# Kernel tuning notes

Hardware: AMD Instinct MI355X
Metric: run time of the kernel (lower is better)

## Reference

```python
import jax, jax.numpy as jnp
import numpy as np

N_NODES = 100000
N_EDGES = 3200000
N_FEAT = 128
DIM = 64
N_GRAPHS = 4096
EPS = 1e-5


def setup_inputs() -> dict:
    key = jax.random.key(0)
    ks = jax.random.split(key, 20)
    x = jax.random.normal(ks[0], (N_NODES, N_FEAT), dtype=jnp.float32)
    edge_index = jax.random.randint(ks[1], (2, N_EDGES), 0, N_NODES, dtype=jnp.int64)
    batch = jnp.sort(jax.random.randint(ks[2], (N_NODES,), 0, N_GRAPHS, dtype=jnp.int64))
    s = 0.1
    inp = {
        "x": x, "edge_index": edge_index, "batch": batch,
        "w1": jax.random.normal(ks[3], (N_FEAT, DIM), jnp.float32) * s,
        "b1": jnp.zeros((DIM,), jnp.float32),
        "bn1_g": 1.0 + s * jax.random.normal(ks[4], (DIM,), jnp.float32),
        "bn1_b": s * jax.random.normal(ks[5], (DIM,), jnp.float32),
        "conv_w": jax.random.normal(ks[6], (3, DIM, DIM), jnp.float32) * s,
        "conv_b": jnp.zeros((3, DIM), jnp.float32),
        "bnc_g": 1.0 + s * jax.random.normal(ks[7], (3, DIM), jnp.float32),
        "bnc_b": s * jax.random.normal(ks[8], (3, DIM), jnp.float32),
        "mlp_w": jax.random.normal(ks[9], (3, DIM, DIM), jnp.float32) * s,
        "mlp_b": jnp.zeros((3, DIM), jnp.float32),
        "bnm_g": 1.0 + s * jax.random.normal(ks[10], (3, DIM), jnp.float32),
        "bnm_b": s * jax.random.normal(ks[11], (3, DIM), jnp.float32),
        "out_w": jax.random.normal(ks[12], (DIM, 1), jnp.float32) * s,
        "out_b": jnp.zeros((1,), jnp.float32),
    }
    return inp


def _batchnorm(h, g, b):
    # training-mode BN: batch stats over the node/graph axis, biased variance
    m = jnp.mean(h, axis=0)
    v = jnp.var(h, axis=0)
    return (h - m) * jax.lax.rsqrt(v + EPS) * g + b


def _forward(x, edge_index, batch, w1, b1, bn1_g, bn1_b, conv_w, conv_b,
             bnc_g, bnc_b, mlp_w, mlp_b, bnm_g, bnm_b, out_w, out_b):
    src, dst = edge_index[0], edge_index[1]
    n = x.shape[0]
    # degree with self-loops (GCNConv default: add_self_loops=True, sym norm)
    deg = jax.ops.segment_sum(jnp.ones((src.shape[0],), x.dtype), dst, num_segments=n) + 1.0
    dis = jax.lax.rsqrt(deg)                  # D^{-1/2}
    enorm = (dis[src] * dis[dst])[:, None]    # per-edge norm [E,1]
    self_norm = (dis * dis)[:, None]          # self-loop norm = 1/deg [N,1]

    def gcn(h, W, b):
        h = h @ W                                                  # lin first (PyG)
        agg = jax.ops.segment_sum(h[src] * enorm, dst, num_segments=n)
        return agg + h * self_norm + b

    h = _batchnorm(jax.nn.relu(gcn(x, w1, b1)), bn1_g, bn1_b)
    for i in range(3):
        h = _batchnorm(gcn(h, conv_w[i], conv_b[i]), bnc_g[i], bnc_b[i])
    p = jax.ops.segment_sum(h, batch, num_segments=N_GRAPHS)       # global_add_pool
    for i in range(3):
        p = _batchnorm(jax.nn.relu(p @ mlp_w[i] + mlp_b[i]), bnm_g[i], bnm_b[i])
        # dropout: eval mode -> identity
    return p @ out_w + out_b


def reference(x, edge_index, batch, w1, b1, bn1_g, bn1_b, conv_w, conv_b,
              bnc_g, bnc_b, mlp_w, mlp_b, bnm_g, bnm_b, out_w, out_b):
    return _forward(x, edge_index, batch, w1, b1, bn1_g, bn1_b, conv_w, conv_b,
                    bnc_g, bnc_b, mlp_w, mlp_b, bnm_g, bnm_b, out_w, out_b)
```

## Files before the change

### kernel.cpp

```cpp
#include <hip/hip_runtime.h>
#include <hip/hip_bf16.h>

#define N_FEAT 128
#define DIM 64


__global__ void hist_kernel(const int* __restrict__ dst, int E, int* __restrict__ cnt) {
    int e = blockIdx.x * blockDim.x + threadIdx.x;
    if (e < E) atomicAdd(&cnt[dst[e]], 1);
}

__global__ void dis_kernel(const int* __restrict__ cnt, float* __restrict__ dis, int N) {
    int i = blockIdx.x * blockDim.x + threadIdx.x;
    if (i < N) dis[i] = rsqrtf((float)cnt[i] + 1.0f);
}

__global__ void scanA_kernel(const int* __restrict__ cnt, int N,
                             int* __restrict__ tmp, int* __restrict__ blk) {
    __shared__ int ts[256];
    int t = threadIdx.x;
    int base = blockIdx.x * 1024 + t * 4;
    int v[4];
    int s = 0;
#pragma unroll
    for (int j = 0; j < 4; j++) {
        int i = base + j;
        v[j] = (i < N) ? cnt[i] : 0;
        s += v[j];
    }
    ts[t] = s;
    __syncthreads();
    for (int off = 1; off < 256; off <<= 1) {
        int x = (t >= off) ? ts[t - off] : 0;
        __syncthreads();
        ts[t] += x;
        __syncthreads();
    }
    int run = ts[t] - s;
#pragma unroll
    for (int j = 0; j < 4; j++) {
        run += v[j];
        int i = base + j;
        if (i < N) tmp[i] = run;
    }
    if (t == 255) blk[blockIdx.x] = ts[255];
}

__global__ void scanB_kernel(int* __restrict__ blk, int nb) {
    __shared__ int ts[128];
    int t = threadIdx.x;
    int v = (t < nb) ? blk[t] : 0;
    ts[t] = v;
    __syncthreads();
    for (int off = 1; off < 128; off <<= 1) {
        int x = (t >= off) ? ts[t - off] : 0;
        __syncthreads();
        ts[t] += x;
        __syncthreads();
    }
    if (t < nb) blk[t] = ts[t] - v;
}

__global__ void scanC_kernel(const int* __restrict__ tmp, const int* __restrict__ blk,
                             int N, int E, int* __restrict__ rowp, int* __restrict__ cur) {
    int i = blockIdx.x * blockDim.x + threadIdx.x;
    if (i < N) {
        int b = i >> 10;
        int local = i & 1023;
        int excl = blk[b] + (local ? tmp[i - 1] : 0);
        rowp[i] = excl;
        cur[i] = excl;
    }
    if (i == 0) rowp[N] = E;
}

__global__ void fill_kernel(const int* __restrict__ src, const int* __restrict__ dst, int E,
                            const float* __restrict__ dis, int* __restrict__ cur,
                            int2* __restrict__ ecw) {
    int e = blockIdx.x * blockDim.x + threadIdx.x;
    if (e < E) {
        int s = src[e], d = dst[e];
        int pos = atomicAdd(&cur[d], 1);
        ecw[pos] = make_int2(s, __float_as_int(dis[s] * dis[d]));
    }
}


template<int K, bool AFFINE, bool BIAS, bool RELU, bool STATS>
__global__ __launch_bounds__(256) void gemm_kernel(
    const float* __restrict__ A, const float* __restrict__ W,
    const float* __restrict__ scale, const float* __restrict__ shift,
    const float* __restrict__ bias, float* __restrict__ C,
    float* __restrict__ stats, int M)
{
    __shared__ float As[64][K + 1];
    __shared__ float Ws[K][64];
    __shared__ float bs[64], bq[64];
    int t = threadIdx.x;
    int row0 = blockIdx.x * 64;

    for (int q = t; q < K * 16; q += 256) {
        int k = q >> 4, c4 = (q & 15) << 2;
        float4 w = *reinterpret_cast<const float4*>(&W[k * 64 + c4]);
        *reinterpret_cast<float4*>(&Ws[k][c4]) = w;
    }
    for (int q = t; q < 64 * (K / 4); q += 256) {
        int r = q / (K / 4);
        int k4 = (q % (K / 4)) * 4;
        int row = row0 + r;
        float4 a;
        if (row < M) {
            a = *reinterpret_cast<const float4*>(&A[(size_t)row * K + k4]);
            if (AFFINE) {
                a.x = a.x * scale[k4]     + shift[k4];
                a.y = a.y * scale[k4 + 1] + shift[k4 + 1];
                a.z = a.z * scale[k4 + 2] + shift[k4 + 2];
                a.w = a.w * scale[k4 + 3] + shift[k4 + 3];
            }
        } else {
            a = make_float4(0.f, 0.f, 0.f, 0.f);
        }
        As[r][k4] = a.x; As[r][k4 + 1] = a.y; As[r][k4 + 2] = a.z; As[r][k4 + 3] = a.w;
    }
    __syncthreads();

    int ty = t >> 4, tx = t & 15;
    int r0 = ty * 4, c0 = tx * 4;
    float acc[4][4] = {};
#pragma unroll 8
    for (int k = 0; k < K; k++) {
        float a0 = As[r0][k], a1 = As[r0 + 1][k], a2 = As[r0 + 2][k], a3 = As[r0 + 3][k];
        float4 w = *reinterpret_cast<const float4*>(&Ws[k][c0]);
        acc[0][0] += a0 * w.x; acc[0][1] += a0 * w.y; acc[0][2] += a0 * w.z; acc[0][3] += a0 * w.w;
        acc[1][0] += a1 * w.x; acc[1][1] += a1 * w.y; acc[1][2] += a1 * w.z; acc[1][3] += a1 * w.w;
        acc[2][0] += a2 * w.x; acc[2][1] += a2 * w.y; acc[2][2] += a2 * w.z; acc[2][3] += a2 * w.w;
        acc[3][0] += a3 * w.x; acc[3][1] += a3 * w.y; acc[3][2] += a3 * w.z; acc[3][3] += a3 * w.w;
    }

    if (STATS) {
        if (t < 64) { bs[t] = 0.f; bq[t] = 0.f; }
        __syncthreads();
    }
    float ssum[4] = {0.f, 0.f, 0.f, 0.f}, ssq[4] = {0.f, 0.f, 0.f, 0.f};
#pragma unroll
    for (int i = 0; i < 4; i++) {
        int row = row0 + r0 + i;
        if (row < M) {
            float4 v;
            float* vp = &v.x;
#pragma unroll
            for (int j = 0; j < 4; j++) {
                float x = acc[i][j];
                if (BIAS) x += bias[c0 + j];
                if (RELU) x = fmaxf(x, 0.f);
                vp[j] = x;
                if (STATS) { ssum[j] += x; ssq[j] += x * x; }
            }
            *reinterpret_cast<float4*>(&C[(size_t)row * 64 + c0]) = v;
        }
    }
    if (STATS) {
#pragma unroll
        for (int j = 0; j < 4; j++) {
            atomicAdd(&bs[c0 + j], ssum[j]);
            atomicAdd(&bq[c0 + j], ssq[j]);
        }
        __syncthreads();
        if (t < 64) {
            atomicAdd(&stats[t], bs[t]);
            atomicAdd(&stats[64 + t], bq[t]);
        }
    }
}


template<bool RELU>
__global__ __launch_bounds__(256) void agg_kernel(
    const float* __restrict__ H, const int* __restrict__ rowp,
    const int2* __restrict__ ecw,
    const float* __restrict__ dis, const float* __restrict__ bias,
    float* __restrict__ Hout, float* __restrict__ stats, int N)
{
    __shared__ float bs[64], bq[64];
    int t = threadIdx.x;
    int lane = t & 63;
    int base = (blockIdx.x * 4 + (t >> 6)) * 8;
    float b = bias[lane];
    float ssum = 0.f, ssq = 0.f;
    for (int u = 0; u < 8; u++) {
        int n = base + u;
        if (n >= N) break;
        int e0 = rowp[n], e1 = rowp[n + 1];
        float acc = 0.f;
        for (int e = e0; e < e1; e += 8) {
            int   idx[8];
            float ww[8];
#pragma unroll
            for (int j = 0; j < 8; j++) {
                int ee = e + j;
                bool ok = ee < e1;
                int2 p = ecw[ok ? ee : e0];
                idx[j] = p.x;
                ww[j]  = ok ? __int_as_float(p.y) : 0.f;
            }
            float h[8];
#pragma unroll
            for (int j = 0; j < 8; j++)
                h[j] = H[(size_t)idx[j] * 64 + lane];
#pragma unroll
            for (int j = 0; j < 8; j++)
                acc += h[j] * ww[j];
        }
        float dn = dis[n];
        acc += H[(size_t)n * 64 + lane] * (dn * dn);
        acc += b;
        if (RELU) acc = fmaxf(acc, 0.f);
        Hout[(size_t)n * 64 + lane] = acc;
        ssum += acc;
        ssq += acc * acc;
    }
    if (t < 64) { bs[t] = 0.f; bq[t] = 0.f; }
    __syncthreads();
    atomicAdd(&bs[lane], ssum);
    atomicAdd(&bq[lane], ssq);
    __syncthreads();
    if (t < 64) {
        atomicAdd(&stats[t], bs[t]);
        atomicAdd(&stats[64 + t], bq[t]);
    }
}


__global__ void bnprep_kernel(const float* __restrict__ stats, const float* __restrict__ g,
                              const float* __restrict__ b, float* __restrict__ ss, float cntInv) {
    int c = threadIdx.x;
    float mean = stats[c] * cntInv;
    float var = stats[64 + c] * cntInv - mean * mean;
    float sc = g[c] * rsqrtf(var + 1e-5f);
    ss[c] = sc;
    ss[64 + c] = b[c] - mean * sc;
}


__global__ __launch_bounds__(256) void pool_kernel(
    const float* __restrict__ H, const int* __restrict__ batch,
    const float* __restrict__ ss, float* __restrict__ P, int N)
{
    int t = threadIdx.x;
    int lane = t & 63;
    int base = (blockIdx.x * 4 + (t >> 6)) * 8;
    float sc = ss[lane], sh = ss[64 + lane];
    float acc = 0.f;
    int gprev = -1;
    for (int u = 0; u < 8; u++) {
        int n = base + u;
        if (n >= N) break;
        int g = batch[n];
        if (g != gprev) {
            if (gprev >= 0) atomicAdd(&P[(size_t)gprev * 64 + lane], acc);
            acc = 0.f;
            gprev = g;
        }
        acc += H[(size_t)n * 64 + lane] * sc + sh;
    }
    if (gprev >= 0) atomicAdd(&P[(size_t)gprev * 64 + lane], acc);
}


__global__ __launch_bounds__(256) void final_kernel(
    const float* __restrict__ P, const float* __restrict__ ss,
    const float* __restrict__ outw, const float* __restrict__ outb,
    float* __restrict__ out, int G)
{
    int t = threadIdx.x;
    int lane = t & 63;
    int g = blockIdx.x * 4 + (t >> 6);
    if (g >= G) return;
    float v = (P[(size_t)g * 64 + lane] * ss[lane] + ss[64 + lane]) * outw[lane];
#pragma unroll
    for (int off = 32; off >= 1; off >>= 1) v += __shfl_xor(v, off, 64);
    if (lane == 0) out[g] = v + outb[0];
}


extern "C" void kernel_launch(void* const* d_in, const int* in_sizes, int n_in,
                              void* d_out, int out_size, void* d_ws, size_t ws_size,
                              hipStream_t stream)
{
    const float* x      = (const float*)d_in[0];
    const int*   ei     = (const int*)d_in[1];
    const int*   batch  = (const int*)d_in[2];
    const float* w1     = (const float*)d_in[3];
    const float* b1     = (const float*)d_in[4];
    const float* bn1_g  = (const float*)d_in[5];
    const float* bn1_b  = (const float*)d_in[6];
    const float* conv_w = (const float*)d_in[7];
    const float* conv_b = (const float*)d_in[8];
    const float* bnc_g  = (const float*)d_in[9];
    const float* bnc_b  = (const float*)d_in[10];
    const float* mlp_w  = (const float*)d_in[11];
    const float* mlp_b  = (const float*)d_in[12];
    const float* bnm_g  = (const float*)d_in[13];
    const float* bnm_b  = (const float*)d_in[14];
    const float* out_w  = (const float*)d_in[15];
    const float* out_b  = (const float*)d_in[16];
    float* out = (float*)d_out;

    const int N = in_sizes[0] / N_FEAT;
    const int E = in_sizes[1] / 2;
    const int G = out_size;
    const int* esrc = ei;
    const int* edst = ei + E;

    char* ws = (char*)d_ws;
    size_t off = 0;
    auto alloc = [&](size_t bytes) {
        size_t cur = off;
        off += (bytes + 255) & ~(size_t)255;
        return (void*)(ws + cur);
    };

    int*   deg   = (int*)alloc((size_t)N * 4);
    float* dis   = (float*)alloc((size_t)N * 4);
    int*   rtmp  = (int*)alloc((size_t)N * 4);
    int*   rowp  = (int*)alloc((size_t)(N + 1) * 4);
    int*   cur   = (int*)alloc((size_t)N * 4);
    int*   blk   = (int*)alloc(256 * 4);
    int2*  ecw   = (int2*)alloc((size_t)E * 8);
    float* bufA  = (float*)alloc((size_t)(N + 64) * 64 * 4);
    float* bufB  = (float*)alloc((size_t)(N + 64) * 64 * 4);
    float* stats = (float*)alloc(7 * 128 * 4);
    float* ssbuf = (float*)alloc(7 * 128 * 4);
    float* P     = (float*)alloc((size_t)G * 64 * 4);
    float* pA    = (float*)alloc((size_t)G * 64 * 4);
    float* pB    = (float*)alloc((size_t)G * 64 * 4);

    hipMemsetAsync(deg, 0, (size_t)N * 4, stream);
    hipMemsetAsync(stats, 0, 7 * 128 * 4, stream);
    hipMemsetAsync(P, 0, (size_t)G * 64 * 4, stream);

    hist_kernel<<<(E + 255) / 256, 256, 0, stream>>>(edst, E, deg);
    dis_kernel<<<(N + 255) / 256, 256, 0, stream>>>(deg, dis, N);
    int nchunk = (N + 1023) / 1024;
    scanA_kernel<<<nchunk, 256, 0, stream>>>(deg, N, rtmp, blk);
    scanB_kernel<<<1, 128, 0, stream>>>(blk, nchunk);
    scanC_kernel<<<(N + 255) / 256, 256, 0, stream>>>(rtmp, blk, N, E, rowp, cur);
    fill_kernel<<<(E + 255) / 256, 256, 0, stream>>>(esrc, edst, E, dis, cur, ecw);

    int gemmN_grid = (N + 63) / 64;
    int aggN_grid = (N + 31) / 32;

    gemm_kernel<128, false, false, false, false><<<gemmN_grid, 256, 0, stream>>>(
        x, w1, nullptr, nullptr, nullptr, bufA, nullptr, N);
    agg_kernel<true><<<aggN_grid, 256, 0, stream>>>(
        bufA, rowp, ecw, dis, b1, bufB, stats, N);
    bnprep_kernel<<<1, 64, 0, stream>>>(stats, bn1_g, bn1_b, ssbuf, 1.0f / N);

    for (int i = 0; i < 3; i++) {
        const float* W  = conv_w + (size_t)i * 64 * 64;
        const float* bb = conv_b + (size_t)i * 64;
        float* st     = stats + (size_t)(1 + i) * 128;
        float* ss_in  = ssbuf + (size_t)i * 128;
        float* ss_out = ssbuf + (size_t)(1 + i) * 128;
        gemm_kernel<64, true, false, false, false><<<gemmN_grid, 256, 0, stream>>>(
            bufB, W, ss_in, ss_in + 64, nullptr, bufA, nullptr, N);
        agg_kernel<false><<<aggN_grid, 256, 0, stream>>>(
            bufA, rowp, ecw, dis, bb, bufB, st, N);
        bnprep_kernel<<<1, 64, 0, stream>>>(st, bnc_g + (size_t)i * 64, bnc_b + (size_t)i * 64,
                                            ss_out, 1.0f / N);
    }

    pool_kernel<<<aggN_grid, 256, 0, stream>>>(bufB, batch, ssbuf + 3 * 128, P, N);

    int gemmG_grid = (G + 63) / 64;
    gemm_kernel<64, false, true, true, true><<<gemmG_grid, 256, 0, stream>>>(
        P, mlp_w, nullptr, nullptr, mlp_b, pA, stats + 4 * 128, G);
    bnprep_kernel<<<1, 64, 0, stream>>>(stats + 4 * 128, bnm_g, bnm_b, ssbuf + 4 * 128, 1.0f / G);

    gemm_kernel<64, true, true, true, true><<<gemmG_grid, 256, 0, stream>>>(
        pA, mlp_w + 64 * 64, ssbuf + 4 * 128, ssbuf + 4 * 128 + 64,
        mlp_b + 64, pB, stats + 5 * 128, G);
    bnprep_kernel<<<1, 64, 0, stream>>>(stats + 5 * 128, bnm_g + 64, bnm_b + 64, ssbuf + 5 * 128, 1.0f / G);

    gemm_kernel<64, true, true, true, true><<<gemmG_grid, 256, 0, stream>>>(
        pB, mlp_w + 2 * 64 * 64, ssbuf + 5 * 128, ssbuf + 5 * 128 + 64,
        mlp_b + 2 * 64, pA, stats + 6 * 128, G);
    bnprep_kernel<<<1, 64, 0, stream>>>(stats + 6 * 128, bnm_g + 2 * 64, bnm_b + 2 * 64, ssbuf + 6 * 128, 1.0f / G);

    final_kernel<<<(G + 3) / 4, 256, 0, stream>>>(pA, ssbuf + 6 * 128, out_w, out_b, out, G);
}
```

Before: 1.218 ms.

## Pad CSR rows to multiples of eight and prescale indices for branchless aggregation

Each CSR row's degree is rounded up to a multiple of 8, and a new pad kernel fills the tail slots with zero-weight entries pointing at row 0. Source indices are stored pre-shifted to byte offsets. This lets the aggregation loop drop its per-edge bounds checks and index multiply, at the cost of extra padded edge traffic and a larger edge buffer. The GEMM also reads shared-memory A tiles as float4, with padding changed to K+4, which reduces the number of LDS loads.

```diff
diff --git a/kernel.cpp b/kernel.cpp
--- a/kernel.cpp
+++ b/kernel.cpp
@@ -25,7 +25,7 @@
 #pragma unroll
     for (int j = 0; j < 4; j++) {
         int i = base + j;
-        v[j] = (i < N) ? cnt[i] : 0;
+        v[j] = (i < N) ? ((cnt[i] + 7) & ~7) : 0;
         s += v[j];
     }
     ts[t] = s;
@@ -62,7 +62,8 @@
 }
 
 __global__ void scanC_kernel(const int* __restrict__ tmp, const int* __restrict__ blk,
-                             int N, int E, int* __restrict__ rowp, int* __restrict__ cur) {
+                             const int* __restrict__ cnt,
+                             int N, int* __restrict__ rowp, int* __restrict__ cur) {
     int i = blockIdx.x * blockDim.x + threadIdx.x;
     if (i < N) {
         int b = i >> 10;
@@ -70,8 +71,8 @@
         int excl = blk[b] + (local ? tmp[i - 1] : 0);
         rowp[i] = excl;
         cur[i] = excl;
-    }
-    if (i == 0) rowp[N] = E;
+        if (i == N - 1) rowp[N] = excl + ((cnt[i] + 7) & ~7);
+    }
 }
 
 __global__ void fill_kernel(const int* __restrict__ src, const int* __restrict__ dst, int E,
@@ -81,7 +82,16 @@
     if (e < E) {
         int s = src[e], d = dst[e];
         int pos = atomicAdd(&cur[d], 1);
-        ecw[pos] = make_int2(s, __float_as_int(dis[s] * dis[d]));
+        ecw[pos] = make_int2(s << 8, __float_as_int(dis[s] * dis[d]));
+    }
+}
+
+__global__ void pad_kernel(const int* __restrict__ cur, const int* __restrict__ rowp,
+                           int2* __restrict__ ecw, int N) {
+    int i = blockIdx.x * blockDim.x + threadIdx.x;
+    if (i < N) {
+        int p = cur[i], e = rowp[i + 1];
+        for (; p < e; p++) ecw[p] = make_int2(0, 0);
     }
 }
 
@@ -93,7 +103,7 @@
     const float* __restrict__ bias, float* __restrict__ C,
     float* __restrict__ stats, int M)
 {
-    __shared__ float As[64][K + 1];
+    __shared__ float As[64][K + 4];
     __shared__ float Ws[K][64];
     __shared__ float bs[64], bq[64];
     int t = threadIdx.x;
@@ -120,21 +130,32 @@
         } else {
             a = make_float4(0.f, 0.f, 0.f, 0.f);
         }
-        As[r][k4] = a.x; As[r][k4 + 1] = a.y; As[r][k4 + 2] = a.z; As[r][k4 + 3] = a.w;
+        *reinterpret_cast<float4*>(&As[r][k4]) = a;
     }
     __syncthreads();
 
     int ty = t >> 4, tx = t & 15;
     int r0 = ty * 4, c0 = tx * 4;
     float acc[4][4] = {};
-#pragma unroll 8
-    for (int k = 0; k < K; k++) {
-        float a0 = As[r0][k], a1 = As[r0 + 1][k], a2 = As[r0 + 2][k], a3 = As[r0 + 3][k];
-        float4 w = *reinterpret_cast<const float4*>(&Ws[k][c0]);
-        acc[0][0] += a0 * w.x; acc[0][1] += a0 * w.y; acc[0][2] += a0 * w.z; acc[0][3] += a0 * w.w;
-        acc[1][0] += a1 * w.x; acc[1][1] += a1 * w.y; acc[1][2] += a1 * w.z; acc[1][3] += a1 * w.w;
-        acc[2][0] += a2 * w.x; acc[2][1] += a2 * w.y; acc[2][2] += a2 * w.z; acc[2][3] += a2 * w.w;
-        acc[3][0] += a3 * w.x; acc[3][1] += a3 * w.y; acc[3][2] += a3 * w.z; acc[3][3] += a3 * w.w;
+#pragma unroll 2
+    for (int k = 0; k < K; k += 4) {
+        float4 A0 = *reinterpret_cast<const float4*>(&As[r0 + 0][k]);
+        float4 A1 = *reinterpret_cast<const float4*>(&As[r0 + 1][k]);
+        float4 A2 = *reinterpret_cast<const float4*>(&As[r0 + 2][k]);
+        float4 A3 = *reinterpret_cast<const float4*>(&As[r0 + 3][k]);
+        float ar[4][4] = {{A0.x, A0.y, A0.z, A0.w}, {A1.x, A1.y, A1.z, A1.w},
+                          {A2.x, A2.y, A2.z, A2.w}, {A3.x, A3.y, A3.z, A3.w}};
+#pragma unroll
+        for (int kk = 0; kk < 4; kk++) {
+            float4 w = *reinterpret_cast<const float4*>(&Ws[k + kk][c0]);
+#pragma unroll
+            for (int i = 0; i < 4; i++) {
+                acc[i][0] += ar[i][kk] * w.x;
+                acc[i][1] += ar[i][kk] * w.y;
+                acc[i][2] += ar[i][kk] * w.z;
+                acc[i][3] += ar[i][kk] * w.w;
+            }
+        }
     }
 
     if (STATS) {
@@ -184,6 +205,8 @@
     __shared__ float bs[64], bq[64];
     int t = threadIdx.x;
     int lane = t & 63;
+    unsigned lane4 = (unsigned)lane << 2;
+    const char* Hb = (const char*)H;
     int base = (blockIdx.x * 4 + (t >> 6)) * 8;
     float b = bias[lane];
     float ssum = 0.f, ssq = 0.f;
@@ -193,23 +216,16 @@
         int e0 = rowp[n], e1 = rowp[n + 1];
         float acc = 0.f;
         for (int e = e0; e < e1; e += 8) {
-            int   idx[8];
-            float ww[8];
-#pragma unroll
-            for (int j = 0; j < 8; j++) {
-                int ee = e + j;
-                bool ok = ee < e1;
-                int2 p = ecw[ok ? ee : e0];
-                idx[j] = p.x;
-                ww[j]  = ok ? __int_as_float(p.y) : 0.f;
-            }
+            int2 p[8];
+#pragma unroll
+            for (int j = 0; j < 8; j++) p[j] = ecw[e + j];
             float h[8];
 #pragma unroll
             for (int j = 0; j < 8; j++)
-                h[j] = H[(size_t)idx[j] * 64 + lane];
+                h[j] = *(const float*)(Hb + ((unsigned)p[j].x + lane4));
 #pragma unroll
             for (int j = 0; j < 8; j++)
-                acc += h[j] * ww[j];
+                acc += h[j] * __int_as_float(p[j].y);
         }
         float dn = dis[n];
         acc += H[(size_t)n * 64 + lane] * (dn * dn);
@@ -326,7 +342,7 @@
     int*   rowp  = (int*)alloc((size_t)(N + 1) * 4);
     int*   cur   = (int*)alloc((size_t)N * 4);
     int*   blk   = (int*)alloc(256 * 4);
-    int2*  ecw   = (int2*)alloc((size_t)E * 8);
+    int2*  ecw   = (int2*)alloc(((size_t)E + 8ull * N) * 8);
     float* bufA  = (float*)alloc((size_t)(N + 64) * 64 * 4);
     float* bufB  = (float*)alloc((size_t)(N + 64) * 64 * 4);
     float* stats = (float*)alloc(7 * 128 * 4);
@@ -344,8 +360,9 @@
     int nchunk = (N + 1023) / 1024;
     scanA_kernel<<<nchunk, 256, 0, stream>>>(deg, N, rtmp, blk);
     scanB_kernel<<<1, 128, 0, stream>>>(blk, nchunk);
-    scanC_kernel<<<(N + 255) / 256, 256, 0, stream>>>(rtmp, blk, N, E, rowp, cur);
+    scanC_kernel<<<(N + 255) / 256, 256, 0, stream>>>(rtmp, blk, deg, N, rowp, cur);
     fill_kernel<<<(E + 255) / 256, 256, 0, stream>>>(esrc, edst, E, dis, cur, ecw);
+    pad_kernel<<<(N + 255) / 256, 256, 0, stream>>>(cur, rowp, ecw, N);
 
     int gemmN_grid = (N + 63) / 64;
     int aggN_grid = (N + 31) / 32;
```

After: 1.171 ms. 3.9% less time.
